# Performance work log

Hardware: AMD Instinct MI355X
Metric: run time of the kernel (lower is better)

The kernel has to match this reference:

```python
import jax, jax.numpy as jnp
import numpy as np

TOKENS, D_IN, FEATURES = 8192, 4096, 16384


def setup_inputs() -> dict:
    key = jax.random.key(0)
    k1, k2, k3, k4 = jax.random.split(key, 4)
    inputs = jax.random.normal(k1, (TOKENS, D_IN), dtype=jnp.float32)
    # int4-valued kernel stored as int32 (values in [0, 8) stand in for int4 codes)
    kernel = jax.random.randint(k2, (D_IN, FEATURES), 0, 8, dtype=jnp.int32)
    # per-output-channel scale; keep strictly positive to avoid div-by-zero
    scale = jax.random.uniform(k3, (1, FEATURES), dtype=jnp.float32) + 0.5
    bias = jax.random.normal(k4, (FEATURES,), dtype=jnp.float32)
    return {"inputs": inputs, "kernel": kernel, "scale": scale, "bias": bias}


def reference(inputs, kernel, scale, bias):
    # Dequantize int4 kernel: upcast + per-channel scale division, then GEMM.
    w = kernel.astype(inputs.dtype) / scale          # [D_IN, FEATURES]
    y = inputs @ w                                   # [TOKENS, FEATURES]
    return y + bias
```

## Files before the change

### kernel.cpp

```cpp
#include <hip/hip_runtime.h>

#define TOKENS 8192
#define D_IN   4096
#define FEATS  16384
#define NT     (D_IN / 128)
#define NIT    (NT / 2)

typedef __attribute__((ext_vector_type(4))) int   i4v;
typedef __attribute__((ext_vector_type(4))) float f32x4;

__device__ __forceinline__ void gload_lds16(const void* g, void* l) {
  __builtin_amdgcn_global_load_lds(
      (const __attribute__((address_space(1))) void*)g,
      (__attribute__((address_space(3))) void*)l, 16, 0, 0);
}

__device__ __forceinline__ int pack4(float4 f, float inv) {
  int a = __float2int_rn(f.x * inv), b = __float2int_rn(f.y * inv),
      c = __float2int_rn(f.z * inv), d = __float2int_rn(f.w * inv);
  return (a & 0xff) | ((b & 0xff) << 8) | ((c & 0xff) << 16) | ((d & 0xff) << 24);
}

__global__ __launch_bounds__(256) void quant_x_kernel(const float* __restrict__ x,
                                                      signed char* __restrict__ xq,
                                                      float* __restrict__ xs) {
  const int row = blockIdx.x, t = threadIdx.x;
  const float* xr = x + (long)row * D_IN;
  float4 v0 = *(const float4*)(xr + t * 16 + 0);
  float4 v1 = *(const float4*)(xr + t * 16 + 4);
  float4 v2 = *(const float4*)(xr + t * 16 + 8);
  float4 v3 = *(const float4*)(xr + t * 16 + 12);
  float m = 0.f;
  m = fmaxf(m, fmaxf(fmaxf(fabsf(v0.x), fabsf(v0.y)), fmaxf(fabsf(v0.z), fabsf(v0.w))));
  m = fmaxf(m, fmaxf(fmaxf(fabsf(v1.x), fabsf(v1.y)), fmaxf(fabsf(v1.z), fabsf(v1.w))));
  m = fmaxf(m, fmaxf(fmaxf(fabsf(v2.x), fabsf(v2.y)), fmaxf(fabsf(v2.z), fabsf(v2.w))));
  m = fmaxf(m, fmaxf(fmaxf(fabsf(v3.x), fabsf(v3.y)), fmaxf(fabsf(v3.z), fabsf(v3.w))));
#pragma unroll
  for (int off = 32; off >= 1; off >>= 1) m = fmaxf(m, __shfl_xor(m, off));
  __shared__ float wm[4];
  if ((t & 63) == 0) wm[t >> 6] = m;
  __syncthreads();
  m = fmaxf(fmaxf(wm[0], wm[1]), fmaxf(wm[2], wm[3]));
  m = fmaxf(m, 1e-20f);
  const float inv = 127.f / m;
  if (t == 0) xs[row] = m / 127.f;
  int4 o;
  o.x = pack4(v0, inv); o.y = pack4(v1, inv);
  o.z = pack4(v2, inv); o.w = pack4(v3, inv);
  *(int4*)(xq + (long)row * D_IN + t * 16) = o;
}

__global__ __launch_bounds__(256) void wtrans8_kernel(const int* __restrict__ kq,
                                                      signed char* __restrict__ wt) {
  __shared__ signed char tile[64][68];
  const int n0 = blockIdx.x * 64, k0 = blockIdx.y * 64;
  const int t = threadIdx.x;
  const int kr = t >> 4, nc = (t & 15) * 4;
#pragma unroll
  for (int p = 0; p < 4; p++) {
    int4 v = *(const int4*)(kq + (long)(k0 + kr + 16 * p) * FEATS + n0 + nc);
    tile[kr + 16 * p][nc + 0] = (signed char)v.x;
    tile[kr + 16 * p][nc + 1] = (signed char)v.y;
    tile[kr + 16 * p][nc + 2] = (signed char)v.z;
    tile[kr + 16 * p][nc + 3] = (signed char)v.w;
  }
  __syncthreads();
  const int nr = t >> 4, kc = (t & 15) * 4;
#pragma unroll
  for (int p = 0; p < 4; p++) {
    int n = nr + 16 * p;
    int o = (tile[kc + 0][n] & 0xff) | ((tile[kc + 1][n] & 0xff) << 8) |
            ((tile[kc + 2][n] & 0xff) << 16) | ((tile[kc + 3][n] & 0xff) << 24);
    *(int*)(wt + (long)(n0 + n) * D_IN + k0 + kc) = o;
  }
}

#define BAR        __builtin_amdgcn_s_barrier()
#define WAIT_LGKM  asm volatile("s_waitcnt lgkmcnt(0)" ::: "memory")
#define VMCNT6     asm volatile("s_waitcnt vmcnt(6)" ::: "memory")
#define VMCNT0     asm volatile("s_waitcnt vmcnt(0)" ::: "memory")
#define PRIO1      __builtin_amdgcn_s_setprio(1)
#define PRIO0      __builtin_amdgcn_s_setprio(0)

#define STAGE_A(B_, R0, KT) do { if ((KT) < NT) \
  gload_lds16(Xq + (m0 + (R0) + sr) * (long)D_IN + (long)(KT) * 128 + sgb, \
              (char*)&lds[B_][0][0] + (R0) * 128 + wid * 1024); } while (0)
#define STAGE_B(B_, R0, KT) do { if ((KT) < NT) \
  gload_lds16(Wq + (n0 + (R0) + sr) * (long)D_IN + (long)(KT) * 128 + sgb, \
              (char*)&lds[B_][1][0] + (R0) * 128 + wid * 1024); } while (0)

#define LDA1(B_, I) do { \
  const char* _p = (const char*)&lds[B_][0][0] + (wr * 128 + (I) * 16 + rl) * 128; \
  aF[(I) & 3][0] = *(const i4v*)(_p + koff0); \
  aF[(I) & 3][1] = *(const i4v*)(_p + koff1); } while (0)
#define LDA4(B_, H) do { LDA1(B_, (H)*4+0); LDA1(B_, (H)*4+1); LDA1(B_, (H)*4+2); LDA1(B_, (H)*4+3); } while (0)
#define LDB1(B_, J) do { \
  const char* _p = (const char*)&lds[B_][1][0] + (wc * 64 + (J) * 16 + rl) * 128; \
  bF[J][0] = *(const i4v*)(_p + koff0); \
  bF[J][1] = *(const i4v*)(_p + koff1); } while (0)
#define LDB4(B_) do { LDB1(B_, 0); LDB1(B_, 1); LDB1(B_, 2); LDB1(B_, 3); } while (0)

#define MM1(I, J, KS) \
  acc[I][J] = __builtin_amdgcn_mfma_i32_16x16x64_i8(aF[(I) & 3][KS], bF[J][KS], acc[I][J], 0, 0, 0)
#define MM16(H, JH) do { \
  MM1((H)*4+0,(JH)*2+0,0); MM1((H)*4+0,(JH)*2+0,1); \
  MM1((H)*4+0,(JH)*2+1,0); MM1((H)*4+0,(JH)*2+1,1); \
  MM1((H)*4+1,(JH)*2+0,0); MM1((H)*4+1,(JH)*2+0,1); \
  MM1((H)*4+1,(JH)*2+1,0); MM1((H)*4+1,(JH)*2+1,1); \
  MM1((H)*4+2,(JH)*2+0,0); MM1((H)*4+2,(JH)*2+0,1); \
  MM1((H)*4+2,(JH)*2+1,0); MM1((H)*4+2,(JH)*2+1,1); \
  MM1((H)*4+3,(JH)*2+0,0); MM1((H)*4+3,(JH)*2+0,1); \
  MM1((H)*4+3,(JH)*2+1,0); MM1((H)*4+3,(JH)*2+1,1); } while (0)

__global__ __launch_bounds__(512, 2) void gemm8i_kernel(
    const signed char* __restrict__ Xq,
    const signed char* __restrict__ Wq,
    const float* __restrict__ xs,
    const float* __restrict__ scale,
    const float* __restrict__ bias,
    float* __restrict__ C) {
  __shared__ __attribute__((aligned(16))) signed char lds[2][2][256 * 128];

  const int tid = threadIdx.x;
  const int lane = tid & 63, wid = tid >> 6;
  const int wr = wid >> 2, wc = wid & 3;
  const int rl = lane & 15, q = lane >> 4;

  const int bid = blockIdx.x;
  const int swz = (bid & 7) * 256 + (bid >> 3);
  const long m0 = (long)(swz >> 6) * 256;
  const long n0 = (long)(swz & 63) * 256;

  const int sr = tid >> 3;
  const int sgb = ((tid & 7) ^ (sr & 7)) * 16;

  const int xm = (rl & 7) << 4;
  const int koff0 = (q * 16) ^ xm;
  const int koff1 = (64 + q * 16) ^ xm;

  i4v acc[8][4] = {};
  i4v aF[4][2], bF[4][2];

  STAGE_B(0, 0, 0); STAGE_B(0, 64, 0); STAGE_B(0, 128, 0); STAGE_B(0, 192, 0);
  STAGE_A(0, 0, 0); STAGE_A(0, 64, 0); STAGE_A(0, 128, 0); STAGE_A(0, 192, 0);
  STAGE_B(1, 0, 1); STAGE_B(1, 64, 1); STAGE_B(1, 128, 1); STAGE_B(1, 192, 1);
  STAGE_A(1, 0, 1); STAGE_A(1, 128, 1);
  VMCNT6;
  BAR;

  for (int it = 0; it < NIT; ++it) {
    const int t1 = 2 * it + 1, t2 = 2 * it + 2, t3 = 2 * it + 3;
    LDA4(0, 0); LDB4(0);
    STAGE_A(1, 64, t1); STAGE_A(1, 192, t1);
    WAIT_LGKM; PRIO1; MM16(0, 0); PRIO0;
    BAR;
    STAGE_B(0, 0, t2); STAGE_B(0, 64, t2);
    PRIO1; MM16(0, 1); PRIO0;
    BAR;
    LDA4(0, 1);
    STAGE_B(0, 128, t2); STAGE_B(0, 192, t2);
    WAIT_LGKM; PRIO1; MM16(1, 0); PRIO0;
    BAR;
    STAGE_A(0, 0, t2); STAGE_A(0, 128, t2);
    PRIO1; MM16(1, 1); PRIO0;
    if (it == NIT - 1) { VMCNT0; } else { VMCNT6; }
    BAR;
    LDA4(1, 0); LDB4(1);
    STAGE_A(0, 64, t2); STAGE_A(0, 192, t2);
    WAIT_LGKM; PRIO1; MM16(0, 0); PRIO0;
    BAR;
    STAGE_B(1, 0, t3); STAGE_B(1, 64, t3);
    PRIO1; MM16(0, 1); PRIO0;
    BAR;
    LDA4(1, 1);
    STAGE_B(1, 128, t3); STAGE_B(1, 192, t3);
    WAIT_LGKM; PRIO1; MM16(1, 0); PRIO0;
    BAR;
    STAGE_A(1, 0, t3); STAGE_A(1, 128, t3);
    PRIO1; MM16(1, 1); PRIO0;
    VMCNT6;
    BAR;
  }

#pragma unroll
  for (int j = 0; j < 4; j++) {
    const long col = n0 + wc * 64 + j * 16 + rl;
    const float rs = 1.0f / scale[col];
    const float bv = bias[col];
#pragma unroll
    for (int i = 0; i < 8; i++) {
      const long row0 = m0 + wr * 128 + i * 16 + q * 4;
#pragma unroll
      for (int r = 0; r < 4; r++) {
        C[(row0 + r) * (long)FEATS + col] = (float)acc[i][j][r] * xs[row0 + r] * rs + bv;
      }
    }
  }
}

__global__ void naive_kernel(const float* __restrict__ x, const int* __restrict__ kq,
                             const float* __restrict__ scale, const float* __restrict__ bias,
                             float* __restrict__ out) {
  __shared__ float xa[16][16];
  __shared__ float wb[16][17];
  const int n = blockIdx.x * 16 + threadIdx.x;
  const int m = blockIdx.y * 16 + threadIdx.y;
  float accv = 0.f;
  for (int k0 = 0; k0 < D_IN; k0 += 16) {
    xa[threadIdx.y][threadIdx.x] = x[(long)m * D_IN + k0 + threadIdx.x];
    wb[threadIdx.y][threadIdx.x] = (float)kq[(long)(k0 + threadIdx.y) * FEATS + n];
    __syncthreads();
#pragma unroll
    for (int kk = 0; kk < 16; kk++) accv += xa[threadIdx.y][kk] * wb[kk][threadIdx.x];
    __syncthreads();
  }
  out[(long)m * FEATS + n] = accv * (1.0f / scale[n]) + bias[n];
}

extern "C" void kernel_launch(void* const* d_in, const int* in_sizes, int n_in,
                              void* d_out, int out_size, void* d_ws, size_t ws_size,
                              hipStream_t stream) {
  const float* x     = (const float*)d_in[0];
  const int*   kq    = (const int*)d_in[1];
  const float* scale = (const float*)d_in[2];
  const float* bias  = (const float*)d_in[3];
  float* out = (float*)d_out;

  const size_t need = (size_t)TOKENS * D_IN + (size_t)FEATS * D_IN + TOKENS * 4;
  if (ws_size < need) {
    naive_kernel<<<dim3(FEATS / 16, TOKENS / 16), dim3(16, 16), 0, stream>>>(
        x, kq, scale, bias, out);
    return;
  }

  signed char* Xq = (signed char*)d_ws;
  signed char* Wq = Xq + (size_t)TOKENS * D_IN;
  float* xs = (float*)(Wq + (size_t)FEATS * D_IN);

  quant_x_kernel<<<TOKENS, 256, 0, stream>>>(x, Xq, xs);
  wtrans8_kernel<<<dim3(FEATS / 64, D_IN / 64), dim3(256), 0, stream>>>(kq, Wq);
  gemm8i_kernel<<<dim3((TOKENS / 256) * (FEATS / 256)), 512, 0, stream>>>(
      Xq, Wq, xs, scale, bias, out);
}
```

Before: 653.0 us.

## Rework int8 GEMM phase schedule and XCD-aware tile mapping

Splits the B-fragment LDS reads into two halves spread across the MMA phases, reorders the global-to-LDS staging of A and B tiles, and wraps each MMA phase in barriers. It also replaces the block-to-tile swizzle with an XCD-aware mapping: each of the 8 XCDs owns a band of 4 M-tiles and walks N in rectangles of 8 tiles, which is meant to improve L2 reuse. The extra barriers per phase add synchronization cost, and the reordered staging has to stay consistent with the vmcnt accounting.

```diff
diff --git a/kernel.cpp b/kernel.cpp
--- a/kernel.cpp
+++ b/kernel.cpp
@@ -98,7 +98,7 @@
   const char* _p = (const char*)&lds[B_][1][0] + (wc * 64 + (J) * 16 + rl) * 128; \
   bF[J][0] = *(const i4v*)(_p + koff0); \
   bF[J][1] = *(const i4v*)(_p + koff1); } while (0)
-#define LDB4(B_) do { LDB1(B_, 0); LDB1(B_, 1); LDB1(B_, 2); LDB1(B_, 3); } while (0)
+#define LDB2(B_, P) do { LDB1(B_, (P)*2+0); LDB1(B_, (P)*2+1); } while (0)
 
 #define MM1(I, J, KS) \
   acc[I][J] = __builtin_amdgcn_mfma_i32_16x16x64_i8(aF[(I) & 3][KS], bF[J][KS], acc[I][J], 0, 0, 0)
@@ -126,10 +126,15 @@
   const int wr = wid >> 2, wc = wid & 3;
   const int rl = lane & 15, q = lane >> 4;
 
-  const int bid = blockIdx.x;
-  const int swz = (bid & 7) * 256 + (bid >> 3);
-  const long m0 = (long)(swz >> 6) * 256;
-  const long n0 = (long)(swz & 63) * 256;
+  const int bid  = blockIdx.x;
+  const int xcd  = bid & 7;
+  const int l    = bid >> 3;
+  const int rect = l >> 5;
+  const int r    = l & 31;
+  const int mloc = r & 3;
+  const int nl   = r >> 2;
+  const long m0 = (long)(xcd * 4 + mloc) * 256;
+  const long n0 = (long)(rect * 8 + nl) * 256;
 
   const int sr = tid >> 3;
   const int sgb = ((tid & 7) ^ (sr & 7)) * 16;
@@ -150,34 +155,30 @@
 
   for (int it = 0; it < NIT; ++it) {
     const int t1 = 2 * it + 1, t2 = 2 * it + 2, t3 = 2 * it + 3;
-    LDA4(0, 0); LDB4(0);
+    LDA4(0, 0); LDB2(0, 0);
     STAGE_A(1, 64, t1); STAGE_A(1, 192, t1);
-    WAIT_LGKM; PRIO1; MM16(0, 0); PRIO0;
-    BAR;
+    BAR; WAIT_LGKM; PRIO1; MM16(0, 0); PRIO0; BAR;
+    LDB2(0, 1);
+    STAGE_A(0, 0, t2); STAGE_A(0, 128, t2);
+    BAR; WAIT_LGKM; PRIO1; MM16(0, 1); PRIO0; BAR;
+    LDA4(0, 1);
     STAGE_B(0, 0, t2); STAGE_B(0, 64, t2);
-    PRIO1; MM16(0, 1); PRIO0;
-    BAR;
-    LDA4(0, 1);
+    BAR; WAIT_LGKM; PRIO1; MM16(1, 0); PRIO0; BAR;
     STAGE_B(0, 128, t2); STAGE_B(0, 192, t2);
-    WAIT_LGKM; PRIO1; MM16(1, 0); PRIO0;
-    BAR;
-    STAGE_A(0, 0, t2); STAGE_A(0, 128, t2);
-    PRIO1; MM16(1, 1); PRIO0;
+    BAR; PRIO1; MM16(1, 1); PRIO0;
     if (it == NIT - 1) { VMCNT0; } else { VMCNT6; }
     BAR;
-    LDA4(1, 0); LDB4(1);
+    LDA4(1, 0); LDB2(1, 0);
     STAGE_A(0, 64, t2); STAGE_A(0, 192, t2);
-    WAIT_LGKM; PRIO1; MM16(0, 0); PRIO0;
-    BAR;
+    BAR; WAIT_LGKM; PRIO1; MM16(0, 0); PRIO0; BAR;
+    LDB2(1, 1);
+    STAGE_A(1, 0, t3); STAGE_A(1, 128, t3);
+    BAR; WAIT_LGKM; PRIO1; MM16(0, 1); PRIO0; BAR;
+    LDA4(1, 1);
     STAGE_B(1, 0, t3); STAGE_B(1, 64, t3);
-    PRIO1; MM16(0, 1); PRIO0;
-    BAR;
-    LDA4(1, 1);
+    BAR; WAIT_LGKM; PRIO1; MM16(1, 0); PRIO0; BAR;
     STAGE_B(1, 128, t3); STAGE_B(1, 192, t3);
-    WAIT_LGKM; PRIO1; MM16(1, 0); PRIO0;
-    BAR;
-    STAGE_A(1, 0, t3); STAGE_A(1, 128, t3);
-    PRIO1; MM16(1, 1); PRIO0;
+    BAR; PRIO1; MM16(1, 1); PRIO0;
     VMCNT6;
     BAR;
   }
@@ -191,8 +192,8 @@
     for (int i = 0; i < 8; i++) {
       const long row0 = m0 + wr * 128 + i * 16 + q * 4;
 #pragma unroll
-      for (int r = 0; r < 4; r++) {
-        C[(row0 + r) * (long)FEATS + col] = (float)acc[i][j][r] * xs[row0 + r] * rs + bv;
+      for (int r2 = 0; r2 < 4; r2++) {
+        C[(row0 + r2) * (long)FEATS + col] = (float)acc[i][j][r2] * xs[row0 + r2] * rs + bv;
       }
     }
   }
```

Result: slower. 696.9 us (+6.7%).
